# Kernel tuning notes

Measured on AMD Instinct MI355X. Metric: run time of the kernel, lower is better.

## Reference

```python
import jax, jax.numpy as jnp
import numpy as np

NH = 16  # num_heads


def _ln(x, eps=1e-6):
    m = x.mean(-1, keepdims=True)
    v = ((x - m) ** 2).mean(-1, keepdims=True)
    return (x - m) * jax.lax.rsqrt(v + eps)


def _mod(z, sh, sc):
    return z * (1 + sc[:, None, :]) + sh[:, None, :]


def _attn(q, k, v, out_w, out_b, nh=NH):
    B, S, E = q.shape
    hd = E // nh
    q = q.reshape(B, S, nh, hd)
    k = k.reshape(B, -1, nh, hd)
    v = v.reshape(B, -1, nh, hd)
    s = jnp.einsum('bqhd,bkhd->bhqk', q, k) / float(np.sqrt(hd))
    a = jax.nn.softmax(s, axis=-1)
    o = jnp.einsum('bhqk,bkhd->bqhd', a, v).reshape(B, S, E)
    return o @ out_w.T + out_b


def setup_inputs() -> dict:
    key = jax.random.key(0)
    ks = jax.random.split(key, 40)
    E, L, Ne, I, p, C, clip, Kd = 1024, 2, 8, 4096, 2, 4, 768, 1536
    N = (64 // p) ** 2
    n = lambda k, shape, s=0.02: (jax.random.normal(k, shape, jnp.float32) * s)
    inp = {
        'x': jax.random.normal(ks[0], (2, C, 64, 64), jnp.float32),
        't': jax.random.uniform(ks[1], (2,), jnp.float32) * 1000.0,
        'clip_vec': jax.random.normal(ks[2], (2, clip), jnp.float32),
        'qwen_context': jax.random.normal(ks[3], (2, 256, Kd), jnp.float32),
        'conv_w': n(ks[4], (E, C, p, p)),
        'conv_b': n(ks[5], (E,)),
        'pos_embed': n(ks[6], (1, N, E)),
        'tmlp_w1': n(ks[7], (256, 256)), 'tmlp_b1': n(ks[8], (256,)),
        'tmlp_w2': n(ks[9], (256, 256)), 'tmlp_b2': n(ks[10], (256,)),
        'cond_w': n(ks[11], (E, 256 + clip)), 'cond_b': n(ks[12], (E,)),
        'ada_w': n(ks[13], (L, 9 * E, E)), 'ada_b': n(ks[14], (L, 9 * E)),
        'sa_in_w': n(ks[15], (L, 3 * E, E)), 'sa_in_b': n(ks[16], (L, 3 * E)),
        'sa_out_w': n(ks[17], (L, E, E)), 'sa_out_b': n(ks[18], (L, E)),
        'ca_q_w': n(ks[19], (L, E, E)), 'ca_k_w': n(ks[20], (L, E, Kd)),
        'ca_v_w': n(ks[21], (L, E, Kd)), 'ca_in_b': n(ks[22], (L, 3 * E)),
        'ca_out_w': n(ks[23], (L, E, E)), 'ca_out_b': n(ks[24], (L, E)),
        'gate_w': n(ks[25], (L, Ne, E)), 'gate_b': n(ks[26], (L, Ne)),
        'e_w1': n(ks[27], (L, Ne, I, E)), 'e_b1': n(ks[28], (L, Ne, I)),
        'e_w2': n(ks[29], (L, Ne, E, I)), 'e_b2': n(ks[30], (L, Ne, E)),
        'fin_w': n(ks[31], (p * p * C, E)), 'fin_b': n(ks[32], (p * p * C,)),
    }
    return inp


def reference(x, t, clip_vec, qwen_context, conv_w, conv_b, pos_embed,
              tmlp_w1, tmlp_b1, tmlp_w2, tmlp_b2, cond_w, cond_b,
              ada_w, ada_b, sa_in_w, sa_in_b, sa_out_w, sa_out_b,
              ca_q_w, ca_k_w, ca_v_w, ca_in_b, ca_out_w, ca_out_b,
              gate_w, gate_b, e_w1, e_b1, e_w2, e_b2, fin_w, fin_b):
    B, C, H, W = x.shape
    E, p = conv_w.shape[0], conv_w.shape[-1]
    h, w = H // p, W // p
    # patch-embed conv (kernel==stride) as unfold + matmul
    patches = x.reshape(B, C, h, p, w, p).transpose(0, 2, 4, 1, 3, 5).reshape(B, h * w, C * p * p)
    xt = patches @ conv_w.reshape(E, -1).T + conv_b + pos_embed
    # sinusoidal timestep embedding (dim 256)
    half = 128
    freqs = jnp.exp(jnp.arange(half, dtype=jnp.float32) * (-np.log(10000.0) / (half - 1)))
    te = t[:, None] * freqs[None, :]
    te = jnp.concatenate([jnp.sin(te), jnp.cos(te)], -1)
    te = jax.nn.silu(te @ tmlp_w1.T + tmlp_b1) @ tmlp_w2.T + tmlp_b2
    c = jnp.concatenate([te, clip_vec], -1) @ cond_w.T + cond_b  # [B,E]
    depth = ada_w.shape[0]
    for i in range(depth):
        pr = jax.nn.silu(c) @ ada_w[i].T + ada_b[i]
        sh_sa, sc_sa, g_sa, sh_ca, sc_ca, g_ca, sh_m, sc_m, g_m = jnp.split(pr, 9, axis=1)
        # self-attention
        xn = _mod(_ln(xt), sh_sa, sc_sa)
        qkv = xn @ sa_in_w[i].T + sa_in_b[i]
        q, k, v = jnp.split(qkv, 3, axis=-1)
        xt = xt + g_sa[:, None, :] * _attn(q, k, v, sa_out_w[i], sa_out_b[i])
        # cross-attention with separate q/k/v projections
        xn = _mod(_ln(xt), sh_ca, sc_ca)
        q = xn @ ca_q_w[i].T + ca_in_b[i, :E]
        k = qwen_context @ ca_k_w[i].T + ca_in_b[i, E:2 * E]
        v = qwen_context @ ca_v_w[i].T + ca_in_b[i, 2 * E:]
        xt = xt + g_ca[:, None, :] * _attn(q, k, v, ca_out_w[i], ca_out_b[i])
        # top-2 sparse MoE (dense-combine formulation: zero weight for unrouted experts)
        xn = _mod(_ln(xt), sh_m, sc_m)
        probs = jax.nn.softmax(xn @ gate_w[i].T + gate_b[i], axis=-1)
        tw, ti = jax.lax.top_k(probs, 2)
        tw = tw / (tw.sum(-1, keepdims=True) + 1e-6)
        wd = (jax.nn.one_hot(ti, probs.shape[-1], dtype=xn.dtype) * tw[..., None]).sum(-2)  # [B,S,Ne]
        hid = jax.nn.gelu(jnp.einsum('bsd,eid->bsei', xn, e_w1[i]) + e_b1[i], approximate=True)
        y = jnp.einsum('bsei,eoi->bseo', hid, e_w2[i]) + e_b2[i]
        moe = jnp.einsum('bseo,bse->bso', y, wd)
        xt = xt + g_m[:, None, :] * moe
    # final layer + unpatchify (nhwpqc->nchpwq)
    xt = _ln(xt) @ fin_w.T + fin_b
    out = xt.reshape(B, h, w, p, p, C).transpose(0, 5, 1, 3, 2, 4).reshape(B, C, h * p, w * p)
    return out
```

## Files before the change

kernel.cpp:

```cpp
#include <hip/hip_runtime.h>
#include <hip/hip_bf16.h>

#define B_ 2
#define S_ 1024
#define E_ 1024
#define NHEAD 16
#define NE 8
#define II 4096
#define KD 1536
#define CLIP_ 768
#define TOK (B_*S_)
#define NSLOTP 5120

typedef short bf16x8 __attribute__((ext_vector_type(8)));
typedef float f32x4 __attribute__((ext_vector_type(4)));

__device__ __forceinline__ float siluf(float x){ return x/(1.f+expf(-x)); }
__device__ __forceinline__ float geluf(float x){
    float x3 = x*x*x;
    return 0.5f*x*(1.f+tanhf(0.7978845608028654f*(x+0.044715f*x3)));
}
__device__ __forceinline__ unsigned short h16(float x){
    union { __hip_bfloat16 b; unsigned short u; } c;
    c.b = __float2bfloat16(x);
    return c.u;
}
__device__ __forceinline__ unsigned pk2(float a, float b){
    return (unsigned)h16(a) | ((unsigned)h16(b)<<16);
}
__device__ __forceinline__ void sp(float a, unsigned& hb, unsigned& lb){
    unsigned short h = h16(a);
    float r = a - __uint_as_float(((unsigned)h)<<16);
    hb = h; lb = h16(r);
}
__device__ __forceinline__ size_t pidx(int row, int k, int K){
    return (((size_t)(row>>4)*(K>>5) + (k>>5))<<9) + (((k>>3)&3)<<7) + ((row&15)<<3) + (k&7);
}
__device__ __forceinline__ void gload16(const unsigned short* g, unsigned short* l){
    __builtin_amdgcn_global_load_lds((const __attribute__((address_space(1))) void*)g,
                                     (__attribute__((address_space(3))) void*)l, 16, 0, 0);
}

union U8 { unsigned u[4]; bf16x8 v; uint4 q; };

__global__ void k_patch_embed(const float* __restrict__ x, const float* __restrict__ cw,
                              const float* __restrict__ cb, const float* __restrict__ pos,
                              float* __restrict__ xt){
    int token = blockIdx.x;
    int b = token >> 10, n = token & 1023;
    int hh = n >> 5, ww = n & 31;
    __shared__ float patch[16];
    int tid = threadIdx.x;
    if (tid < 16){
        int c = tid >> 2, py = (tid >> 1) & 1, px = tid & 1;
        patch[tid] = x[(((size_t)b*4 + c)*64 + hh*2+py)*64 + ww*2+px];
    }
    __syncthreads();
    for (int e = tid; e < E_; e += 256){
        float acc = cb[e];
        #pragma unroll
        for (int j=0;j<16;j++) acc += patch[j]*cw[e*16+j];
        xt[(size_t)token*E_ + e] = acc + pos[(size_t)n*E_ + e];
    }
}

__global__ void k_time_cond(const float* __restrict__ t, const float* __restrict__ clip,
                            const float* __restrict__ w1, const float* __restrict__ b1,
                            const float* __restrict__ w2, const float* __restrict__ b2,
                            const float* __restrict__ cw, const float* __restrict__ cbias,
                            float* __restrict__ silu_c){
    int b = blockIdx.x, tid = threadIdx.x;
    __shared__ float te[256], h1[256], te2[256];
    if (tid < 128){
        float f = expf((float)tid * (-9.210340371976184f/127.f));
        float a = t[b]*f;
        te[tid]     = sinf(a);
        te[tid+128] = cosf(a);
    }
    __syncthreads();
    {
        float acc = b1[tid];
        const float* wr = w1 + (size_t)tid*256;
        for (int k=0;k<256;k++) acc += te[k]*wr[k];
        h1[tid] = siluf(acc);
    }
    __syncthreads();
    {
        float acc = b2[tid];
        const float* wr = w2 + (size_t)tid*256;
        for (int k=0;k<256;k++) acc += h1[k]*wr[k];
        te2[tid] = acc;
    }
    __syncthreads();
    const float* cl = clip + (size_t)b*CLIP_;
    for (int e = tid; e < E_; e += 256){
        float acc = cbias[e];
        const float* wr = cw + (size_t)e*1024;
        for (int k=0;k<256;k++)  acc += te2[k]*wr[k];
        for (int k=0;k<CLIP_;k++) acc += cl[k]*wr[256+k];
        silu_c[b*E_+e] = siluf(acc);
    }
}

__global__ void k_ada2(const float* __restrict__ sic, const float* __restrict__ aw,
                       const float* __restrict__ ab, float* __restrict__ pr){
    int row = blockIdx.x*4 + (threadIdx.x>>6);
    int lane = threadIdx.x & 63;
    const float* w = aw + (size_t)row*1024;
    float a0 = 0.f, a1 = 0.f;
    #pragma unroll
    for (int it=0; it<4; it++){
        int k = it*256 + lane*4;
        float4 wv = *(const float4*)(w+k);
        float4 x0 = *(const float4*)(sic+k);
        float4 x1 = *(const float4*)(sic+1024+k);
        a0 += wv.x*x0.x + wv.y*x0.y + wv.z*x0.z + wv.w*x0.w;
        a1 += wv.x*x1.x + wv.y*x1.y + wv.z*x1.z + wv.w*x1.w;
    }
    #pragma unroll
    for (int off=32; off; off>>=1){ a0 += __shfl_down(a0,off); a1 += __shfl_down(a1,off); }
    if (lane==0){
        float bb = ab[row];
        pr[row] = a0 + bb;
        pr[9*E_ + row] = a1 + bb;
    }
}

template<int PACK>
__global__ void k_ln_mod(const float* __restrict__ src, float* __restrict__ dst32,
                         unsigned short* __restrict__ dsth, unsigned short* __restrict__ dstl,
                         const float* __restrict__ pr, int shc, int scc){
    int token = blockIdx.x, tid = threadIdx.x;
    int b = token >> 10;
    const float* row = src + (size_t)token*E_;
    float4 v = *(const float4*)(row + tid*4);
    float s = v.x+v.y+v.z+v.w;
    float ss = v.x*v.x+v.y*v.y+v.z*v.z+v.w*v.w;
    #pragma unroll
    for (int off=32; off; off>>=1){ s += __shfl_down(s,off); ss += __shfl_down(ss,off); }
    __shared__ float rs_[4], rss_[4];
    int wid = tid >> 6;
    if ((tid&63)==0){ rs_[wid]=s; rss_[wid]=ss; }
    __syncthreads();
    s  = rs_[0]+rs_[1]+rs_[2]+rs_[3];
    ss = rss_[0]+rss_[1]+rss_[2]+rss_[3];
    float mean = s*(1.f/1024.f);
    float rstd = rsqrtf(ss*(1.f/1024.f) - mean*mean + 1e-6f);
    const float* shv = pr + b*9*E_ + shc*E_;
    const float* scv = pr + b*9*E_ + scc*E_;
    int e = tid*4;
    float o[4];
    float4 sc4 = *(const float4*)(scv+e);
    float4 sh4 = *(const float4*)(shv+e);
    o[0] = (v.x-mean)*rstd*(1.f+sc4.x) + sh4.x;
    o[1] = (v.y-mean)*rstd*(1.f+sc4.y) + sh4.y;
    o[2] = (v.z-mean)*rstd*(1.f+sc4.z) + sh4.z;
    o[3] = (v.w-mean)*rstd*(1.f+sc4.w) + sh4.w;
    unsigned hu[2], lu[2];
    {
        unsigned h0,l0,h1,l1;
        sp(o[0],h0,l0); sp(o[1],h1,l1);
        hu[0]=h0|(h1<<16); lu[0]=l0|(l1<<16);
        sp(o[2],h0,l0); sp(o[3],h1,l1);
        hu[1]=h0|(h1<<16); lu[1]=l0|(l1<<16);
    }
    if (PACK){
        size_t base = pidx(token, e, E_);
        *(uint2*)(dsth + base) = make_uint2(hu[0],hu[1]);
        *(uint2*)(dstl + base) = make_uint2(lu[0],lu[1]);
    } else {
        *(float4*)(dst32 + (size_t)token*E_ + e) = make_float4(o[0],o[1],o[2],o[3]);
        *(uint2*)(dsth + (size_t)token*E_ + e) = make_uint2(hu[0],hu[1]);
        *(uint2*)(dstl + (size_t)token*E_ + e) = make_uint2(lu[0],lu[1]);
    }
}

__global__ void k_pack_qwen(const float* __restrict__ q, unsigned short* __restrict__ hp,
                            unsigned short* __restrict__ lp){
    int r = blockIdx.x;
    int k = threadIdx.x*8;
    float f[8];
    *(float4*)(f+0) = *(const float4*)(q + (size_t)r*KD + k);
    *(float4*)(f+4) = *(const float4*)(q + (size_t)r*KD + k + 4);
    U8 H, L;
    #pragma unroll
    for (int i=0;i<4;i++){
        unsigned h0,l0,h1,l1;
        sp(f[2*i],h0,l0); sp(f[2*i+1],h1,l1);
        H.u[i] = h0|(h1<<16); L.u[i] = l0|(l1<<16);
    }
    size_t dst = pidx(r, k, KD);
    *(uint4*)(hp + dst) = H.q;
    *(uint4*)(lp + dst) = L.q;
}

__global__ void k_gather_pack(const unsigned short* __restrict__ xh,
                              const unsigned short* __restrict__ xl,
                              const int* __restrict__ list,
                              unsigned short* __restrict__ oh, unsigned short* __restrict__ ol){
    int s = blockIdx.x;
    int tid = threadIdx.x;
    int token = list[s];
    int k = tid*8;
    size_t src = (size_t)token*E_ + k;
    size_t dst = pidx(s, k, E_);
    *(uint4*)(oh + dst) = *(const uint4*)(xh + src);
    *(uint4*)(ol + dst) = *(const uint4*)(xl + src);
}

template<int NPL>
__global__ void k_pack_w(const float* __restrict__ W, unsigned short* __restrict__ hp,
                         unsigned short* __restrict__ lp, int K){
    int rg = blockIdx.x;
    int t = threadIdx.x;
    int K32 = K>>5;
    for (int k = t*8; k < K; k += 1024){
        size_t bb = (((size_t)rg*K32 + (k>>5))<<9) + (((k>>3)&3)<<7);
        #pragma unroll 4
        for (int r=0;r<16;r++){
            const float* src = W + (size_t)(rg*16 + r)*K + k;
            float f[8];
            *(float4*)(f)   = *(const float4*)src;
            *(float4*)(f+4) = *(const float4*)(src+4);
            U8 H, L;
            #pragma unroll
            for (int i2=0;i2<4;i2++){
                unsigned h0,l0,h1,l1;
                sp(f[2*i2],h0,l0); sp(f[2*i2+1],h1,l1);
                H.u[i2]=h0|(h1<<16); L.u[i2]=l0|(l1<<16);
            }
            *(uint4*)(hp + bb + (r<<3)) = H.q;
            if (NPL==2) *(uint4*)(lp + bb + (r<<3)) = L.q;
        }
    }
}

template<int MOE, int EPI, int TERMS, int SPLITK=1>
__global__ __launch_bounds__(256) void k_mm(
    const unsigned short* __restrict__ Ah, const unsigned short* __restrict__ Al,
    const unsigned short* __restrict__ Bh, const unsigned short* __restrict__ Bl,
    const float* __restrict__ biasp, int bstride,
    void* __restrict__ Cp, void* __restrict__ Cp2, int ldc,
    int M, int N, int K,
    const float* __restrict__ pr, int gch,
    const int* __restrict__ cnt, const int* __restrict__ offs)
{
    constexpr int NPL = (TERMS==3)?2:1;
    constexpr int NB  = 2*NPL*8;
    constexpr int NBW = NB/4;
    int e  = MOE ? blockIdx.z : 0;
    int Mm = MOE ? cnt[e] : M;
    int bm = blockIdx.y*128;
    if (MOE && bm >= Mm) return;
    int o0 = MOE ? offs[e] : 0;
    int nt = gridDim.x / SPLITK;
    int ntile = blockIdx.x % nt;
    int kc0 = blockIdx.x / nt;
    int bn = ntile*128;
    int K32 = K >> 5;
    int kbeg = kc0*(K/SPLITK), kend = kbeg + K/SPLITK;
    const float* bias = biasp + (size_t)e*bstride;

    __shared__ __align__(16) unsigned short LDm[2][NB*512];

    int tid = threadIdx.x, lane = tid&63, wid = tid>>6;
    int wm = wid>>1, wn = wid&1;
    int fr = lane&15, fr4 = (lane>>4)*4;
    int l8 = lane<<3;
    int a16 = ((MOE? o0:0) + bm) >> 4;
    int b16 = bn >> 4;
    size_t eoff = (size_t)e * N * K;

    const unsigned short* gb[NBW];
    #pragma unroll
    for (int i=0;i<NBW;i++){
        int bidx = wid*NBW + i;
        int isB = (bidx >= NPL*8) ? 1 : 0;
        int r = bidx - isB*NPL*8;
        int pl = r>>3, rg = r&7;
        const unsigned short* p;
        size_t rgg;
        if (!isB){ p = (TERMS==3 && pl)? Al : Ah; rgg = (size_t)(a16 + rg); }
        else     { p = ((TERMS==3 && pl)? Bl : Bh) + eoff; rgg = (size_t)(b16 + rg); }
        gb[i] = p + ((rgg*K32)<<9) + l8;
    }

    f32x4 acc[4][4];
    #pragma unroll
    for (int m=0;m<4;m++)
        #pragma unroll
        for (int n=0;n<4;n++) acc[m][n] = (f32x4){0.f,0.f,0.f,0.f};

    {
        int kc = kbeg>>5;
        #pragma unroll
        for (int i=0;i<NBW;i++)
            gload16(gb[i] + ((size_t)kc<<9), &LDm[0][(size_t)(wid*NBW+i)<<9]);
    }
    __syncthreads();
    int cur = 0;
    for (int k0=kbeg; k0<kend; k0+=32){
        bool nxt = (k0+32) < kend;
        if (nxt){
            int kc = (k0+32)>>5;
            #pragma unroll
            for (int i=0;i<NBW;i++)
                gload16(gb[i] + ((size_t)kc<<9), &LDm[cur^1][(size_t)(wid*NBW+i)<<9]);
        }
        bf16x8 ah[4], al[4], bh[4], bl[4];
        #pragma unroll
        for (int m=0;m<4;m++){
            ah[m] = *(const bf16x8*)&LDm[cur][(size_t)((wm*4+m)<<9) + l8];
            if (TERMS==3) al[m] = *(const bf16x8*)&LDm[cur][(size_t)((8+wm*4+m)<<9) + l8];
        }
        #pragma unroll
        for (int n=0;n<4;n++){
            bh[n] = *(const bf16x8*)&LDm[cur][(size_t)((NPL*8 + wn*4+n)<<9) + l8];
            if (TERMS==3) bl[n] = *(const bf16x8*)&LDm[cur][(size_t)((NPL*8+8 + wn*4+n)<<9) + l8];
        }
        #pragma unroll
        for (int m=0;m<4;m++)
            #pragma unroll
            for (int n=0;n<4;n++){
                acc[m][n] = __builtin_amdgcn_mfma_f32_16x16x32_bf16(ah[m], bh[n], acc[m][n], 0, 0, 0);
                if (TERMS==3){
                    acc[m][n] = __builtin_amdgcn_mfma_f32_16x16x32_bf16(ah[m], bl[n], acc[m][n], 0, 0, 0);
                    acc[m][n] = __builtin_amdgcn_mfma_f32_16x16x32_bf16(al[m], bh[n], acc[m][n], 0, 0, 0);
                }
            }
        __syncthreads();
        cur ^= 1;
    }

    #pragma unroll
    for (int m=0;m<4;m++){
        #pragma unroll
        for (int j=0;j<4;j++){
            int row = bm + wm*64 + m*16 + fr4 + j;
            if (EPI != 2 && row >= Mm) continue;
            #pragma unroll
            for (int n=0;n<4;n++){
                int col = bn + wn*64 + n*16 + fr;
                float bv = (SPLITK==1 || kc0==0) ? bias[col] : 0.f;
                float v = acc[m][n][j] + bv;
                if (EPI==0){
                    ((float*)Cp)[(size_t)row*ldc + col] = v;
                } else if (EPI==1){
                    int bb = row >> 10;
                    ((float*)Cp)[(size_t)row*ldc + col] += pr[bb*9*E_ + gch*E_ + col] * v;
                } else if (EPI==2){
                    size_t pi = pidx(o0 + row, col, II);
                    if (TERMS==3){
                        unsigned hb, lb; sp(geluf(v), hb, lb);
                        ((unsigned short*)Cp )[pi] = (unsigned short)hb;
                        ((unsigned short*)Cp2)[pi] = (unsigned short)lb;
                    } else {
                        ((unsigned short*)Cp )[pi] = h16(geluf(v));
                    }
                } else {
                    if (SPLITK==1)
                        ((float*)Cp)[(size_t)(o0+row)*ldc + col] = v;
                    else
                        atomicAdd(&((float*)Cp)[(size_t)(o0+row)*ldc + col], v);
                }
            }
        }
    }
}

__global__ __launch_bounds__(256) void k_attn_m(
    const float* __restrict__ qp, int qstride,
    const float* __restrict__ kp, const float* __restrict__ vp, int kvstride,
    unsigned short* __restrict__ oph, unsigned short* __restrict__ opl,
    int Sq, int Sk, float scale)
{
    __shared__ __align__(16) unsigned short Kh[64*72];
    __shared__ __align__(16) unsigned short Kl[64*72];
    __shared__ __align__(16) unsigned V_i[64*70];
    __shared__ __align__(16) unsigned short P_[4][2][16*72];

    int tid = threadIdx.x, lane = tid & 63, wid = tid >> 6;
    int g = lane >> 4, fr = lane & 15;
    int h = blockIdx.y, b = blockIdx.z;
    int qbase = blockIdx.x*64;

    bf16x8 qh[2], ql[2];
    {
        const float* qr = qp + (size_t)(b*Sq + qbase + wid*16 + fr)*qstride + h*64;
        #pragma unroll
        for (int ds=0; ds<2; ds++){
            float f[8];
            *(float4*)(f+0) = *(const float4*)(qr + ds*32 + g*8);
            *(float4*)(f+4) = *(const float4*)(qr + ds*32 + g*8 + 4);
            U8 uh, ul;
            #pragma unroll
            for (int i=0;i<4;i++){
                unsigned h0,l0,h1,l1;
                sp(f[2*i]*scale, h0,l0); sp(f[2*i+1]*scale, h1,l1);
                uh.u[i] = h0|(h1<<16); ul.u[i] = l0|(l1<<16);
            }
            qh[ds] = uh.v; ql[ds] = ul.v;
        }
    }

    float m_run = -1e30f, l_run = 0.f;
    f32x4 oacc[4];
    #pragma unroll
    for (int dt=0;dt<4;dt++) oacc[dt] = (f32x4){0.f,0.f,0.f,0.f};

    unsigned short* PhW = &P_[wid][0][0];
    unsigned short* PlW = &P_[wid][1][0];

    for (int kt0 = 0; kt0 < Sk; kt0 += 64){
        __syncthreads();
        {
            int srow = tid >> 2, d0 = (tid & 3) << 4;
            size_t grow = (size_t)(b*Sk + kt0 + srow)*kvstride + h*64 + d0;
            {
                const float* srcp = kp + grow;
                float f[16];
                *(float4*)(f+0)  = *(const float4*)(srcp+0);
                *(float4*)(f+4)  = *(const float4*)(srcp+4);
                *(float4*)(f+8)  = *(const float4*)(srcp+8);
                *(float4*)(f+12) = *(const float4*)(srcp+12);
                U8 uh0, uh1, ul0, ul1;
                #pragma unroll
                for (int i=0;i<4;i++){
                    unsigned a0,b0,a1,b1;
                    sp(f[2*i],a0,b0); sp(f[2*i+1],a1,b1);
                    uh0.u[i] = a0|(a1<<16); ul0.u[i] = b0|(b1<<16);
                }
                #pragma unroll
                for (int i=0;i<4;i++){
                    unsigned a0,b0,a1,b1;
                    sp(f[8+2*i],a0,b0); sp(f[8+2*i+1],a1,b1);
                    uh1.u[i] = a0|(a1<<16); ul1.u[i] = b0|(b1<<16);
                }
                int base = srow*72 + d0;
                *(uint4*)&Kh[base]     = uh0.q;
                *(uint4*)&Kh[base + 8] = uh1.q;
                *(uint4*)&Kl[base]     = ul0.q;
                *(uint4*)&Kl[base + 8] = ul1.q;
            }
            {
                const float* srcp = vp + grow;
                float f[16];
                *(float4*)(f+0)  = *(const float4*)(srcp+0);
                *(float4*)(f+4)  = *(const float4*)(srcp+4);
                *(float4*)(f+8)  = *(const float4*)(srcp+8);
                *(float4*)(f+12) = *(const float4*)(srcp+12);
                int base = srow*70 + d0;
                #pragma unroll
                for (int i4=0;i4<4;i4++){
                    U8 u;
                    #pragma unroll
                    for (int i=0;i<4;i++){
                        unsigned hb, lb; sp(f[4*i4+i], hb, lb);
                        u.u[i] = hb | (lb<<16);
                    }
                    *(uint2*)&V_i[base + i4*4]     = make_uint2(u.u[0], u.u[1]);
                    *(uint2*)&V_i[base + i4*4 + 2] = make_uint2(u.u[2], u.u[3]);
                }
            }
        }
        __syncthreads();

        f32x4 st[4];
        #pragma unroll
        for (int kt=0;kt<4;kt++) st[kt] = (f32x4){0.f,0.f,0.f,0.f};
        #pragma unroll
        for (int ds=0; ds<2; ds++){
            #pragma unroll
            for (int kt=0;kt<4;kt++){
                int row = kt*16 + fr;
                int so = row*72 + ds*32 + g*8;
                bf16x8 kh  = *(const bf16x8*)&Kh[so];
                bf16x8 klo = *(const bf16x8*)&Kl[so];
                st[kt] = __builtin_amdgcn_mfma_f32_16x16x32_bf16(kh, qh[ds], st[kt], 0,0,0);
                st[kt] = __builtin_amdgcn_mfma_f32_16x16x32_bf16(kh, ql[ds], st[kt], 0,0,0);
                st[kt] = __builtin_amdgcn_mfma_f32_16x16x32_bf16(klo, qh[ds], st[kt], 0,0,0);
            }
        }

        float pmax = -1e30f;
        #pragma unroll
        for (int kt=0;kt<4;kt++)
            #pragma unroll
            for (int r=0;r<4;r++) pmax = fmaxf(pmax, st[kt][r]);
        pmax = fmaxf(pmax, __shfl_xor(pmax, 16));
        pmax = fmaxf(pmax, __shfl_xor(pmax, 32));
        float mnew = fmaxf(m_run, pmax);
        float p[4][4]; float psum = 0.f;
        #pragma unroll
        for (int kt=0;kt<4;kt++)
            #pragma unroll
            for (int r=0;r<4;r++){ float pv = expf(st[kt][r] - mnew); p[kt][r] = pv; psum += pv; }
        psum += __shfl_xor(psum, 16);
        psum += __shfl_xor(psum, 32);
        float corr = expf(m_run - mnew);
        l_run = l_run*corr + psum;
        m_run = mnew;
        #pragma unroll
        for (int j=0;j<4;j++){
            float cj = __shfl(corr, g*4 + j);
            #pragma unroll
            for (int dt=0;dt<4;dt++) oacc[dt][j] *= cj;
        }

        #pragma unroll
        for (int kt=0;kt<4;kt++){
            unsigned h0,l0,h1,l1,h2,l2,h3,l3;
            sp(p[kt][0],h0,l0); sp(p[kt][1],h1,l1);
            sp(p[kt][2],h2,l2); sp(p[kt][3],h3,l3);
            int base = fr*72 + kt*16 + g*4;
            *(unsigned*)&PhW[base]     = h0|(h1<<16);
            *(unsigned*)&PhW[base + 2] = h2|(h3<<16);
            *(unsigned*)&PlW[base]     = l0|(l1<<16);
            *(unsigned*)&PlW[base + 2] = l2|(l3<<16);
        }

        #pragma unroll
        for (int ks=0; ks<2; ks++){
            int pso = fr*72 + ks*32 + g*8;
            bf16x8 ph = *(const bf16x8*)&PhW[pso];
            bf16x8 pl = *(const bf16x8*)&PlW[pso];
            #pragma unroll
            for (int dt=0; dt<4; dt++){
                unsigned w[8];
                #pragma unroll
                for (int j=0;j<8;j++){
                    int row = ks*32 + g*8 + j;
                    w[j] = V_i[row*70 + dt*16 + fr];
                }
                U8 vh, vl;
                #pragma unroll
                for (int i=0;i<4;i++){
                    vh.u[i] = (w[2*i] & 0xffffu) | (w[2*i+1] << 16);
                    vl.u[i] = (w[2*i] >> 16)     | (w[2*i+1] & 0xffff0000u);
                }
                oacc[dt] = __builtin_amdgcn_mfma_f32_16x16x32_bf16(ph, vh.v, oacc[dt], 0,0,0);
                oacc[dt] = __builtin_amdgcn_mfma_f32_16x16x32_bf16(ph, vl.v, oacc[dt], 0,0,0);
                oacc[dt] = __builtin_amdgcn_mfma_f32_16x16x32_bf16(pl, vh.v, oacc[dt], 0,0,0);
            }
        }
    }

    float linv = 1.f / l_run;
    #pragma unroll
    for (int j=0;j<4;j++){
        float lj = __shfl(linv, g*4 + j);
        int row = b*Sq + qbase + wid*16 + g*4 + j;
        #pragma unroll
        for (int dt=0;dt<4;dt++){
            unsigned hb, lb; sp(oacc[dt][j]*lj, hb, lb);
            int k = h*64 + dt*16 + fr;
            size_t pi = pidx(row, k, E_);
            oph[pi] = (unsigned short)hb;
            opl[pi] = (unsigned short)lb;
        }
    }
}

__global__ void k_route(const float* __restrict__ xn, const float* __restrict__ gw,
                        const float* __restrict__ gb, int* __restrict__ i01,
                        float* __restrict__ w01, int* __restrict__ cnt){
    int token = blockIdx.x, lane = threadIdx.x;
    const float* row = xn + (size_t)token*E_;
    float part[8] = {0,0,0,0,0,0,0,0};
    for (int k = lane; k < E_; k += 64){
        float xv = row[k];
        #pragma unroll
        for (int e=0;e<8;e++) part[e] += xv*gw[e*E_+k];
    }
    #pragma unroll
    for (int e=0;e<8;e++){
        #pragma unroll
        for (int off=32; off; off>>=1) part[e] += __shfl_down(part[e], off);
    }
    if (lane==0){
        float lg[8]; float mx = -1e30f;
        #pragma unroll
        for (int e=0;e<8;e++){ lg[e] = part[e]+gb[e]; if (lg[e]>mx) mx = lg[e]; }
        float sum = 0.f;
        #pragma unroll
        for (int e=0;e<8;e++){ lg[e] = expf(lg[e]-mx); sum += lg[e]; }
        int a0 = 0;
        #pragma unroll
        for (int e=1;e<8;e++) if (lg[e] > lg[a0]) a0 = e;
        int a1 = (a0==0)?1:0;
        #pragma unroll
        for (int e=0;e<8;e++) if (e!=a0 && lg[e] > lg[a1]) a1 = e;
        float p0 = lg[a0]/sum, p1 = lg[a1]/sum;
        float inv = 1.f/(p0+p1+1e-6f);
        i01[token*2+0]=a0; i01[token*2+1]=a1;
        w01[token*2+0]=p0*inv; w01[token*2+1]=p1*inv;
        atomicAdd(&cnt[a0],1); atomicAdd(&cnt[a1],1);
    }
}

__global__ void k_scan(const int* __restrict__ cnt, int* __restrict__ offs, int* __restrict__ curs){
    if (threadIdx.x==0 && blockIdx.x==0){
        int o = 0;
        for (int e=0;e<8;e++){
            offs[e]=o; curs[e]=o;
            o += ((cnt[e]+127)>>7)<<7;
        }
    }
}

__global__ void k_place(const int* __restrict__ i01,
                        int* __restrict__ curs, int* __restrict__ list,
                        int* __restrict__ t2s){
    int t = blockIdx.x*256 + threadIdx.x;
    if (t >= TOK) return;
    #pragma unroll
    for (int s=0;s<2;s++){
        int e = i01[t*2+s];
        int p = atomicAdd(&curs[e],1);
        list[p] = t;
        t2s[t*2+s] = p;
    }
}

__global__ void k_moe_combine2(float* __restrict__ xt, const float* __restrict__ yslot,
                               const int* __restrict__ t2s, const float* __restrict__ w01,
                               const float* __restrict__ pr){
    int idx = blockIdx.x*256 + threadIdx.x;
    int token = idx >> 10, n = idx & 1023;
    int b = token >> 10;
    int s0 = t2s[token*2], s1 = t2s[token*2+1];
    float mo = w01[token*2]*yslot[(size_t)s0*E_+n] + w01[token*2+1]*yslot[(size_t)s1*E_+n];
    xt[idx] += pr[b*9*E_ + 8*E_ + n]*mo;
}

__global__ void k_final(const float* __restrict__ xt, const float* __restrict__ fw,
                        const float* __restrict__ fb, float* __restrict__ out){
    int token = blockIdx.x, tid = threadIdx.x;
    int b = token >> 10, n = token & 1023, hh = n >> 5, ww = n & 31;
    const float* row = xt + (size_t)token*E_;
    float4 v = *(const float4*)(row + tid*4);
    float s = v.x+v.y+v.z+v.w;
    float ss = v.x*v.x+v.y*v.y+v.z*v.z+v.w*v.w;
    #pragma unroll
    for (int off=32; off; off>>=1){ s += __shfl_down(s,off); ss += __shfl_down(ss,off); }
    __shared__ float rs_[4], rss_[4];
    int wid = tid >> 6;
    if ((tid&63)==0){ rs_[wid]=s; rss_[wid]=ss; }
    __syncthreads();
    s  = rs_[0]+rs_[1]+rs_[2]+rs_[3];
    ss = rss_[0]+rss_[1]+rss_[2]+rss_[3];
    float mean = s*(1.f/1024.f);
    float rstd = rsqrtf(ss*(1.f/1024.f) - mean*mean + 1e-6f);
    __shared__ float xl[1024];
    int e = tid*4;
    xl[e+0]=(v.x-mean)*rstd; xl[e+1]=(v.y-mean)*rstd;
    xl[e+2]=(v.z-mean)*rstd; xl[e+3]=(v.w-mean)*rstd;
    __syncthreads();
    int o = tid & 15, seg = tid >> 4;
    float part = 0.f;
    const float* wr = fw + (size_t)o*E_ + seg*64;
    const float* xr = xl + seg*64;
    #pragma unroll 8
    for (int j=0;j<64;j++) part += xr[j]*wr[j];
    __shared__ float ps[16][17];
    ps[seg][o] = part;
    __syncthreads();
    if (tid < 16){
        float acc = fb[tid];
        #pragma unroll
        for (int s2=0;s2<16;s2++) acc += ps[s2][tid];
        int py = tid>>3, px = (tid>>2)&1, ch = tid&3;
        out[(((size_t)b*4+ch)*64 + hh*2+py)*64 + ww*2+px] = acc;
    }
}

extern "C" void kernel_launch(void* const* d_in, const int* in_sizes, int n_in,
                              void* d_out, int out_size, void* d_ws, size_t ws_size,
                              hipStream_t stream){
    const float* x        = (const float*)d_in[0];
    const float* t        = (const float*)d_in[1];
    const float* clip     = (const float*)d_in[2];
    const float* qwen     = (const float*)d_in[3];
    const float* conv_w   = (const float*)d_in[4];
    const float* conv_b   = (const float*)d_in[5];
    const float* pos      = (const float*)d_in[6];
    const float* tw1      = (const float*)d_in[7];
    const float* tb1      = (const float*)d_in[8];
    const float* tw2      = (const float*)d_in[9];
    const float* tb2      = (const float*)d_in[10];
    const float* cond_w   = (const float*)d_in[11];
    const float* cond_b   = (const float*)d_in[12];
    const float* ada_w    = (const float*)d_in[13];
    const float* ada_b    = (const float*)d_in[14];
    const float* sa_in_w  = (const float*)d_in[15];
    const float* sa_in_b  = (const float*)d_in[16];
    const float* sa_out_w = (const float*)d_in[17];
    const float* sa_out_b = (const float*)d_in[18];
    const float* ca_q_w   = (const float*)d_in[19];
    const float* ca_k_w   = (const float*)d_in[20];
    const float* ca_v_w   = (const float*)d_in[21];
    const float* ca_in_b  = (const float*)d_in[22];
    const float* ca_out_w = (const float*)d_in[23];
    const float* ca_out_b = (const float*)d_in[24];
    const float* gate_w   = (const float*)d_in[25];
    const float* gate_b   = (const float*)d_in[26];
    const float* e_w1     = (const float*)d_in[27];
    const float* e_b1     = (const float*)d_in[28];
    const float* e_w2     = (const float*)d_in[29];
    const float* e_b2     = (const float*)d_in[30];
    const float* fin_w    = (const float*)d_in[31];
    const float* fin_b    = (const float*)d_in[32];

    float* ws    = (float*)d_ws;
    float* xt    = ws;
    float* xn    = ws + 2097152;
    float* qkv   = ws + 4194304;
    float* yslot = qkv;
    unsigned short* xnh  = (unsigned short*)(ws + 10485760);
    unsigned short* xnl  = (unsigned short*)(ws + 11534336);
    unsigned short* obh  = (unsigned short*)(ws + 12582912);
    unsigned short* obl  = (unsigned short*)(ws + 13631488);
    unsigned short* xnsh = (unsigned short*)(ws + 14680064);
    unsigned short* xnsl = (unsigned short*)(ws + 17301504);
    unsigned short* hidh = (unsigned short*)(ws + 19922944);
    unsigned short* hidl = (unsigned short*)(ws + 30408704);
    unsigned short* qwph = (unsigned short*)(ws + 40894464);
    unsigned short* qwpl = (unsigned short*)(ws + 41287680);
    float* kbuf  = ws + 41680896;
    float* vbuf  = ws + 42205184;
    float* pr    = ws + 42729472;
    float* sic   = ws + 42747904;
    float* w01   = ws + 42749952;
    int*   i01   = (int*)(ws + 42754048);
    int*   t2s   = (int*)(ws + 42758144);
    int*   list  = (int*)(ws + 42762240);
    int*   cnt   = (int*)(ws + 42767360);
    int*   offs  = cnt + 8;
    int*   curs  = cnt + 16;
    unsigned short* wb = (unsigned short*)(ws + 42768384);

    const size_t SA_IN_H=0, SA_IN_L=3145728, SA_OUT_H=6291456, SA_OUT_L=7340032;
    const size_t CAQ_H=8388608, CAQ_L=9437184, CAK_H=10485760, CAK_L=12058624;
    const size_t CAV_H=13631488, CAV_L=15204352, CAO_H=16777216, CAO_L=17825792;
    const size_t W_H=0, W_L=16777216;

    k_patch_embed<<<TOK,256,0,stream>>>(x, conv_w, conv_b, pos, xt);
    k_time_cond<<<B_,256,0,stream>>>(t, clip, tw1, tb1, tw2, tb2, cond_w, cond_b, sic);
    k_pack_qwen<<<B_*256,192,0,stream>>>(qwen, qwph, qwpl);

    for (int i=0;i<2;i++){
        k_ada2<<<2304,256,0,stream>>>(sic, ada_w + (size_t)i*9*E_*E_,
                                      ada_b + (size_t)i*9*E_, pr);
        k_pack_w<2><<<192,128,0,stream>>>(sa_in_w + (size_t)i*3*E_*E_, wb+SA_IN_H, wb+SA_IN_L, E_);
        k_pack_w<2><<<64,128,0,stream>>>(sa_out_w + (size_t)i*E_*E_, wb+SA_OUT_H, wb+SA_OUT_L, E_);
        k_pack_w<2><<<64,128,0,stream>>>(ca_q_w + (size_t)i*E_*E_, wb+CAQ_H, wb+CAQ_L, E_);
        k_pack_w<2><<<64,128,0,stream>>>(ca_k_w + (size_t)i*E_*KD, wb+CAK_H, wb+CAK_L, KD);
        k_pack_w<2><<<64,128,0,stream>>>(ca_v_w + (size_t)i*E_*KD, wb+CAV_H, wb+CAV_L, KD);
        k_pack_w<2><<<64,128,0,stream>>>(ca_out_w + (size_t)i*E_*E_, wb+CAO_H, wb+CAO_L, E_);
        k_ln_mod<1><<<TOK,256,0,stream>>>(xt, nullptr, xnh, xnl, pr, 0, 1);
        k_mm<0,0,3><<<dim3(24,16),256,0,stream>>>(
            xnh, xnl, wb+SA_IN_H, wb+SA_IN_L, sa_in_b + (size_t)i*3*E_, 0,
            qkv, nullptr, 3*E_, TOK, 3*E_, E_, nullptr, 0, nullptr, nullptr);
        k_attn_m<<<dim3(16,NHEAD,B_),256,0,stream>>>(qkv, 3*E_, qkv+E_, qkv+2*E_, 3*E_,
                                                     obh, obl, S_, S_, 0.125f);
        k_mm<0,1,3><<<dim3(8,16),256,0,stream>>>(
            obh, obl, wb+SA_OUT_H, wb+SA_OUT_L, sa_out_b + (size_t)i*E_, 0,
            xt, nullptr, E_, TOK, E_, E_, pr, 2, nullptr, nullptr);
        k_ln_mod<1><<<TOK,256,0,stream>>>(xt, nullptr, xnh, xnl, pr, 3, 4);
        k_mm<0,0,3><<<dim3(8,16),256,0,stream>>>(
            xnh, xnl, wb+CAQ_H, wb+CAQ_L, ca_in_b + (size_t)i*3*E_, 0,
            qkv, nullptr, E_, TOK, E_, E_, nullptr, 0, nullptr, nullptr);
        k_mm<0,0,3><<<dim3(8,4),256,0,stream>>>(
            qwph, qwpl, wb+CAK_H, wb+CAK_L, ca_in_b + (size_t)i*3*E_ + E_, 0,
            kbuf, nullptr, E_, B_*256, E_, KD, nullptr, 0, nullptr, nullptr);
        k_mm<0,0,3><<<dim3(8,4),256,0,stream>>>(
            qwph, qwpl, wb+CAV_H, wb+CAV_L, ca_in_b + (size_t)i*3*E_ + 2*E_, 0,
            vbuf, nullptr, E_, B_*256, E_, KD, nullptr, 0, nullptr, nullptr);
        k_attn_m<<<dim3(16,NHEAD,B_),256,0,stream>>>(qkv, E_, kbuf, vbuf, E_,
                                                     obh, obl, S_, 256, 0.125f);
        k_mm<0,1,3><<<dim3(8,16),256,0,stream>>>(
            obh, obl, wb+CAO_H, wb+CAO_L, ca_out_b + (size_t)i*E_, 0,
            xt, nullptr, E_, TOK, E_, E_, pr, 5, nullptr, nullptr);
        k_ln_mod<0><<<TOK,256,0,stream>>>(xt, xn, xnh, xnl, pr, 6, 7);
        hipMemsetAsync(cnt, 0, 8*sizeof(int), stream);
        hipMemsetAsync(list, 0, NSLOTP*sizeof(int), stream);
        k_route<<<TOK,64,0,stream>>>(xn, gate_w + (size_t)i*NE*E_, gate_b + (size_t)i*NE,
                                     i01, w01, cnt);
        k_scan<<<1,64,0,stream>>>(cnt, offs, curs);
        k_place<<<TOK/256,256,0,stream>>>(i01, curs, list, t2s);
        k_gather_pack<<<NSLOTP,128,0,stream>>>(xnh, xnl, list, xnsh, xnsl);
        hipMemsetAsync(yslot, 0, (size_t)NSLOTP*E_*sizeof(float), stream);
        for (int e0=0;e0<NE;e0+=4){
            if (i==0){
                k_pack_w<2><<<1024,128,0,stream>>>(e_w1 + ((size_t)i*NE+e0)*II*E_, wb+W_H, wb+W_L, E_);
                k_mm<1,2,3><<<dim3(32,32,4),256,0,stream>>>(
                    xnsh, xnsl, wb+W_H, wb+W_L, e_b1 + (size_t)i*NE*II + (size_t)e0*II, II,
                    hidh, hidl, II, 0, II, E_, nullptr, 0, cnt+e0, offs+e0);
            } else {
                k_pack_w<1><<<1024,128,0,stream>>>(e_w1 + ((size_t)i*NE+e0)*II*E_, wb+W_H, nullptr, E_);
                k_mm<1,2,1><<<dim3(32,32,4),256,0,stream>>>(
                    xnsh, nullptr, wb+W_H, nullptr, e_b1 + (size_t)i*NE*II + (size_t)e0*II, II,
                    hidh, nullptr, II, 0, II, E_, nullptr, 0, cnt+e0, offs+e0);
            }
        }
        for (int e0=0;e0<NE;e0+=4){
            if (i==0){
                k_pack_w<2><<<256,128,0,stream>>>(e_w2 + ((size_t)i*NE+e0)*E_*II, wb+W_H, wb+W_L, II);
                k_mm<1,3,3,4><<<dim3(32,32,4),256,0,stream>>>(
                    hidh, hidl, wb+W_H, wb+W_L, e_b2 + (size_t)i*NE*E_ + (size_t)e0*E_, E_,
                    yslot, nullptr, E_, 0, E_, II, nullptr, 0, cnt+e0, offs+e0);
            } else {
                k_pack_w<1><<<256,128,0,stream>>>(e_w2 + ((size_t)i*NE+e0)*E_*II, wb+W_H, nullptr, II);
                k_mm<1,3,1,4><<<dim3(32,32,4),256,0,stream>>>(
                    hidh, nullptr, wb+W_H, nullptr, e_b2 + (size_t)i*NE*E_ + (size_t)e0*E_, E_,
                    yslot, nullptr, E_, 0, E_, II, nullptr, 0, cnt+e0, offs+e0);
            }
        }
        k_moe_combine2<<<TOK*E_/256,256,0,stream>>>(xt, yslot, t2s, w01, pr);
    }
    k_final<<<TOK,256,0,stream>>>(xt, fin_w, fin_b, (float*)d_out);
}
```

Before: 2.407 ms.

## Emit attention K/V pre-split in head-major layout from GEMM epilogues

The QKV and cross-attention K/V projection GEMMs now write K and V directly as hi/lo bf16 splits in a per-head contiguous layout through new epilogues. The attention kernel then loads them with plain vector copies instead of converting fp32 rows on every tile load. The conditioning matvec moves out of a 2-block kernel into a wave-per-output kernel with many blocks. The layer-1 MoE launches all 8 experts in one pack plus one GEMM per stage instead of two chunks. The cost is a larger packed-weight buffer and more complex epilogue index math.

```diff
diff --git a/kernel.cpp b/kernel.cpp
--- a/kernel.cpp
+++ b/kernel.cpp
@@ -64,13 +64,12 @@
     }
 }
 
-__global__ void k_time_cond(const float* __restrict__ t, const float* __restrict__ clip,
-                            const float* __restrict__ w1, const float* __restrict__ b1,
-                            const float* __restrict__ w2, const float* __restrict__ b2,
-                            const float* __restrict__ cw, const float* __restrict__ cbias,
-                            float* __restrict__ silu_c){
+__global__ void k_time_mlp(const float* __restrict__ t,
+                           const float* __restrict__ w1, const float* __restrict__ b1,
+                           const float* __restrict__ w2, const float* __restrict__ b2,
+                           float* __restrict__ te2g){
     int b = blockIdx.x, tid = threadIdx.x;
-    __shared__ float te[256], h1[256], te2[256];
+    __shared__ float te[256], h1[256];
     if (tid < 128){
         float f = expf((float)tid * (-9.210340371976184f/127.f));
         float a = t[b]*f;
@@ -89,17 +88,25 @@
         float acc = b2[tid];
         const float* wr = w2 + (size_t)tid*256;
         for (int k=0;k<256;k++) acc += h1[k]*wr[k];
-        te2[tid] = acc;
-    }
-    __syncthreads();
-    const float* cl = clip + (size_t)b*CLIP_;
-    for (int e = tid; e < E_; e += 256){
-        float acc = cbias[e];
-        const float* wr = cw + (size_t)e*1024;
-        for (int k=0;k<256;k++)  acc += te2[k]*wr[k];
-        for (int k=0;k<CLIP_;k++) acc += cl[k]*wr[256+k];
-        silu_c[b*E_+e] = siluf(acc);
-    }
+        te2g[b*256+tid] = acc;
+    }
+}
+
+__global__ void k_cond(const float* __restrict__ te2g, const float* __restrict__ clip,
+                       const float* __restrict__ cw, const float* __restrict__ cb,
+                       float* __restrict__ silu_c){
+    int idx = blockIdx.x*4 + (threadIdx.x>>6);
+    int lane = threadIdx.x & 63;
+    int b = idx >> 10, e = idx & 1023;
+    const float* wr = cw + (size_t)e*1024;
+    float acc = 0.f;
+    for (int k=lane; k<1024; k+=64){
+        float xv = (k<256)? te2g[b*256+k] : clip[b*CLIP_ + k-256];
+        acc += xv*wr[k];
+    }
+    #pragma unroll
+    for (int off=32; off; off>>=1) acc += __shfl_down(acc,off);
+    if (lane==0) silu_c[b*E_+e] = siluf(acc + cb[e]);
 }
 
 __global__ void k_ada2(const float* __restrict__ sic, const float* __restrict__ aw,
@@ -240,8 +247,8 @@
     const unsigned short* __restrict__ Ah, const unsigned short* __restrict__ Al,
     const unsigned short* __restrict__ Bh, const unsigned short* __restrict__ Bl,
     const float* __restrict__ biasp, int bstride,
-    void* __restrict__ Cp, void* __restrict__ Cp2, int ldc,
-    int M, int N, int K,
+    void* __restrict__ Cp, void* __restrict__ Cp2, void* __restrict__ Cp3, void* __restrict__ Cp4,
+    int ldc, int M, int N, int K,
     const float* __restrict__ pr, int gch,
     const int* __restrict__ cnt, const int* __restrict__ offs)
 {
@@ -357,11 +364,39 @@
                     } else {
                         ((unsigned short*)Cp )[pi] = h16(geluf(v));
                     }
-                } else {
+                } else if (EPI==3){
                     if (SPLITK==1)
                         ((float*)Cp)[(size_t)(o0+row)*ldc + col] = v;
                     else
                         atomicAdd(&((float*)Cp)[(size_t)(o0+row)*ldc + col], v);
+                } else if (EPI==4){
+                    if (col < 1024){
+                        ((float*)Cp)[(size_t)row*1024 + col] = v;
+                    } else {
+                        int c2 = col - 1024;
+                        int isv = c2 >> 10;
+                        int cc = c2 & 1023;
+                        int hh2 = cc >> 6, d = cc & 63;
+                        size_t idx = (((size_t)(row>>10)*NHEAD + hh2)*1024 + (row & 1023))*64 + d;
+                        unsigned hb, lb; sp(v, hb, lb);
+                        if (!isv){
+                            ((unsigned short*)Cp2)[idx] = (unsigned short)hb;
+                            ((unsigned short*)Cp3)[idx] = (unsigned short)lb;
+                        } else {
+                            ((unsigned*)Cp4)[idx] = hb | (lb<<16);
+                        }
+                    }
+                } else if (EPI==5){
+                    int hh2 = col >> 6, d = col & 63;
+                    size_t idx = (((size_t)(row>>8)*NHEAD + hh2)*256 + (row & 255))*64 + d;
+                    unsigned hb, lb; sp(v, hb, lb);
+                    ((unsigned short*)Cp )[idx] = (unsigned short)hb;
+                    ((unsigned short*)Cp2)[idx] = (unsigned short)lb;
+                } else {
+                    int hh2 = col >> 6, d = col & 63;
+                    size_t idx = (((size_t)(row>>8)*NHEAD + hh2)*256 + (row & 255))*64 + d;
+                    unsigned hb, lb; sp(v, hb, lb);
+                    ((unsigned*)Cp)[idx] = hb | (lb<<16);
                 }
             }
         }
@@ -370,7 +405,8 @@
 
 __global__ __launch_bounds__(256) void k_attn_m(
     const float* __restrict__ qp, int qstride,
-    const float* __restrict__ kp, const float* __restrict__ vp, int kvstride,
+    const unsigned short* __restrict__ Khp, const unsigned short* __restrict__ Klp,
+    const unsigned* __restrict__ Vip,
     unsigned short* __restrict__ oph, unsigned short* __restrict__ opl,
     int Sq, int Sk, float scale)
 {
@@ -383,6 +419,7 @@
     int g = lane >> 4, fr = lane & 15;
     int h = blockIdx.y, b = blockIdx.z;
     int qbase = blockIdx.x*64;
+    size_t bhbase = (size_t)(b*NHEAD + h)*Sk*64;
 
     bf16x8 qh[2], ql[2];
     {
@@ -415,52 +452,19 @@
         __syncthreads();
         {
             int srow = tid >> 2, d0 = (tid & 3) << 4;
-            size_t grow = (size_t)(b*Sk + kt0 + srow)*kvstride + h*64 + d0;
-            {
-                const float* srcp = kp + grow;
-                float f[16];
-                *(float4*)(f+0)  = *(const float4*)(srcp+0);
-                *(float4*)(f+4)  = *(const float4*)(srcp+4);
-                *(float4*)(f+8)  = *(const float4*)(srcp+8);
-                *(float4*)(f+12) = *(const float4*)(srcp+12);
-                U8 uh0, uh1, ul0, ul1;
-                #pragma unroll
-                for (int i=0;i<4;i++){
-                    unsigned a0,b0,a1,b1;
-                    sp(f[2*i],a0,b0); sp(f[2*i+1],a1,b1);
-                    uh0.u[i] = a0|(a1<<16); ul0.u[i] = b0|(b1<<16);
-                }
-                #pragma unroll
-                for (int i=0;i<4;i++){
-                    unsigned a0,b0,a1,b1;
-                    sp(f[8+2*i],a0,b0); sp(f[8+2*i+1],a1,b1);
-                    uh1.u[i] = a0|(a1<<16); ul1.u[i] = b0|(b1<<16);
-                }
-                int base = srow*72 + d0;
-                *(uint4*)&Kh[base]     = uh0.q;
-                *(uint4*)&Kh[base + 8] = uh1.q;
-                *(uint4*)&Kl[base]     = ul0.q;
-                *(uint4*)&Kl[base + 8] = ul1.q;
-            }
-            {
-                const float* srcp = vp + grow;
-                float f[16];
-                *(float4*)(f+0)  = *(const float4*)(srcp+0);
-                *(float4*)(f+4)  = *(const float4*)(srcp+4);
-                *(float4*)(f+8)  = *(const float4*)(srcp+8);
-                *(float4*)(f+12) = *(const float4*)(srcp+12);
-                int base = srow*70 + d0;
-                #pragma unroll
-                for (int i4=0;i4<4;i4++){
-                    U8 u;
-                    #pragma unroll
-                    for (int i=0;i<4;i++){
-                        unsigned hb, lb; sp(f[4*i4+i], hb, lb);
-                        u.u[i] = hb | (lb<<16);
-                    }
-                    *(uint2*)&V_i[base + i4*4]     = make_uint2(u.u[0], u.u[1]);
-                    *(uint2*)&V_i[base + i4*4 + 2] = make_uint2(u.u[2], u.u[3]);
-                }
+            size_t gidx = bhbase + (size_t)(kt0 + srow)*64 + d0;
+            int base = srow*72 + d0;
+            *(uint4*)&Kh[base]   = *(const uint4*)(Khp + gidx);
+            *(uint4*)&Kh[base+8] = *(const uint4*)(Khp + gidx + 8);
+            *(uint4*)&Kl[base]   = *(const uint4*)(Klp + gidx);
+            *(uint4*)&Kl[base+8] = *(const uint4*)(Klp + gidx + 8);
+            const unsigned* vsrc = Vip + gidx;
+            int vb = srow*70 + d0;
+            #pragma unroll
+            for (int i4=0;i4<4;i4++){
+                uint4 u = *(const uint4*)(vsrc + i4*4);
+                *(uint2*)&V_i[vb + i4*4]     = make_uint2(u.x,u.y);
+                *(uint2*)&V_i[vb + i4*4 + 2] = make_uint2(u.z,u.w);
             }
         }
         __syncthreads();
@@ -714,8 +718,11 @@
     float* ws    = (float*)d_ws;
     float* xt    = ws;
     float* xn    = ws + 2097152;
-    float* qkv   = ws + 4194304;
-    float* yslot = qkv;
+    float* qbuf  = ws + 4194304;
+    unsigned short* Khp = (unsigned short*)(ws + 6291456);
+    unsigned short* Klp = (unsigned short*)(ws + 7340032);
+    unsigned*       Vip = (unsigned*)(ws + 8388608);
+    float* yslot = ws + 4194304;
     unsigned short* xnh  = (unsigned short*)(ws + 10485760);
     unsigned short* xnl  = (unsigned short*)(ws + 11534336);
     unsigned short* obh  = (unsigned short*)(ws + 12582912);
@@ -726,8 +733,6 @@
     unsigned short* hidl = (unsigned short*)(ws + 30408704);
     unsigned short* qwph = (unsigned short*)(ws + 40894464);
     unsigned short* qwpl = (unsigned short*)(ws + 41287680);
-    float* kbuf  = ws + 41680896;
-    float* vbuf  = ws + 42205184;
     float* pr    = ws + 42729472;
     float* sic   = ws + 42747904;
     float* w01   = ws + 42749952;
@@ -737,6 +742,7 @@
     int*   cnt   = (int*)(ws + 42767360);
     int*   offs  = cnt + 8;
     int*   curs  = cnt + 16;
+    float* te2g  = ws + 42767872;
     unsigned short* wb = (unsigned short*)(ws + 42768384);
 
     const size_t SA_IN_H=0, SA_IN_L=3145728, SA_OUT_H=6291456, SA_OUT_L=7340032;
@@ -745,7 +751,8 @@
     const size_t W_H=0, W_L=16777216;
 
     k_patch_embed<<<TOK,256,0,stream>>>(x, conv_w, conv_b, pos, xt);
-    k_time_cond<<<B_,256,0,stream>>>(t, clip, tw1, tb1, tw2, tb2, cond_w, cond_b, sic);
+    k_time_mlp<<<B_,256,0,stream>>>(t, tw1, tb1, tw2, tb2, te2g);
+    k_cond<<<512,256,0,stream>>>(te2g, clip, cond_w, cond_b, sic);
     k_pack_qwen<<<B_*256,192,0,stream>>>(qwen, qwph, qwpl);
 
     for (int i=0;i<2;i++){
@@ -758,29 +765,29 @@
         k_pack_w<2><<<64,128,0,stream>>>(ca_v_w + (size_t)i*E_*KD, wb+CAV_H, wb+CAV_L, KD);
         k_pack_w<2><<<64,128,0,stream>>>(ca_out_w + (size_t)i*E_*E_, wb+CAO_H, wb+CAO_L, E_);
         k_ln_mod<1><<<TOK,256,0,stream>>>(xt, nullptr, xnh, xnl, pr, 0, 1);
-        k_mm<0,0,3><<<dim3(24,16),256,0,stream>>>(
+        k_mm<0,4,3><<<dim3(24,16),256,0,stream>>>(
             xnh, xnl, wb+SA_IN_H, wb+SA_IN_L, sa_in_b + (size_t)i*3*E_, 0,
-            qkv, nullptr, 3*E_, TOK, 3*E_, E_, nullptr, 0, nullptr, nullptr);
-        k_attn_m<<<dim3(16,NHEAD,B_),256,0,stream>>>(qkv, 3*E_, qkv+E_, qkv+2*E_, 3*E_,
+            qbuf, Khp, Klp, Vip, 0, TOK, 3*E_, E_, nullptr, 0, nullptr, nullptr);
+        k_attn_m<<<dim3(16,NHEAD,B_),256,0,stream>>>(qbuf, E_, Khp, Klp, Vip,
                                                      obh, obl, S_, S_, 0.125f);
         k_mm<0,1,3><<<dim3(8,16),256,0,stream>>>(
             obh, obl, wb+SA_OUT_H, wb+SA_OUT_L, sa_out_b + (size_t)i*E_, 0,
-            xt, nullptr, E_, TOK, E_, E_, pr, 2, nullptr, nullptr);
+            xt, nullptr, nullptr, nullptr, E_, TOK, E_, E_, pr, 2, nullptr, nullptr);
         k_ln_mod<1><<<TOK,256,0,stream>>>(xt, nullptr, xnh, xnl, pr, 3, 4);
         k_mm<0,0,3><<<dim3(8,16),256,0,stream>>>(
             xnh, xnl, wb+CAQ_H, wb+CAQ_L, ca_in_b + (size_t)i*3*E_, 0,
-            qkv, nullptr, E_, TOK, E_, E_, nullptr, 0, nullptr, nullptr);
-        k_mm<0,0,3><<<dim3(8,4),256,0,stream>>>(
+            qbuf, nullptr, nullptr, nullptr, E_, TOK, E_, E_, nullptr, 0, nullptr, nullptr);
+        k_mm<0,5,3><<<dim3(8,4),256,0,stream>>>(
             qwph, qwpl, wb+CAK_H, wb+CAK_L, ca_in_b + (size_t)i*3*E_ + E_, 0,
-            kbuf, nullptr, E_, B_*256, E_, KD, nullptr, 0, nullptr, nullptr);
-        k_mm<0,0,3><<<dim3(8,4),256,0,stream>>>(
+            Khp, Klp, nullptr, nullptr, 0, B_*256, E_, KD, nullptr, 0, nullptr, nullptr);
+        k_mm<0,6,3><<<dim3(8,4),256,0,stream>>>(
             qwph, qwpl, wb+CAV_H, wb+CAV_L, ca_in_b + (size_t)i*3*E_ + 2*E_, 0,
-            vbuf, nullptr, E_, B_*256, E_, KD, nullptr, 0, nullptr, nullptr);
-        k_attn_m<<<dim3(16,NHEAD,B_),256,0,stream>>>(qkv, E_, kbuf, vbuf, E_,
+            Vip, nullptr, nullptr, nullptr, 0, B_*256, E_, KD, nullptr, 0, nullptr, nullptr);
+        k_attn_m<<<dim3(16,NHEAD,B_),256,0,stream>>>(qbuf, E_, Khp, Klp, Vip,
                                                      obh, obl, S_, 256, 0.125f);
         k_mm<0,1,3><<<dim3(8,16),256,0,stream>>>(
             obh, obl, wb+CAO_H, wb+CAO_L, ca_out_b + (size_t)i*E_, 0,
-            xt, nullptr, E_, TOK, E_, E_, pr, 5, nullptr, nullptr);
+            xt, nullptr, nullptr, nullptr, E_, TOK, E_, E_, pr, 5, nullptr, nullptr);
         k_ln_mod<0><<<TOK,256,0,stream>>>(xt, xn, xnh, xnl, pr, 6, 7);
         hipMemsetAsync(cnt, 0, 8*sizeof(int), stream);
         hipMemsetAsync(list, 0, NSLOTP*sizeof(int), stream);
@@ -790,31 +797,28 @@
         k_place<<<TOK/256,256,0,stream>>>(i01, curs, list, t2s);
         k_gather_pack<<<NSLOTP,128,0,stream>>>(xnh, xnl, list, xnsh, xnsl);
         hipMemsetAsync(yslot, 0, (size_t)NSLOTP*E_*sizeof(float), stream);
-        for (int e0=0;e0<NE;e0+=4){
-            if (i==0){
+        if (i==0){
+            for (int e0=0;e0<NE;e0+=4){
                 k_pack_w<2><<<1024,128,0,stream>>>(e_w1 + ((size_t)i*NE+e0)*II*E_, wb+W_H, wb+W_L, E_);
                 k_mm<1,2,3><<<dim3(32,32,4),256,0,stream>>>(
                     xnsh, xnsl, wb+W_H, wb+W_L, e_b1 + (size_t)i*NE*II + (size_t)e0*II, II,
-                    hidh, hidl, II, 0, II, E_, nullptr, 0, cnt+e0, offs+e0);
-            } else {
-                k_pack_w<1><<<1024,128,0,stream>>>(e_w1 + ((size_t)i*NE+e0)*II*E_, wb+W_H, nullptr, E_);
-                k_mm<1,2,1><<<dim3(32,32,4),256,0,stream>>>(
-                    xnsh, nullptr, wb+W_H, nullptr, e_b1 + (size_t)i*NE*II + (size_t)e0*II, II,
-                    hidh, nullptr, II, 0, II, E_, nullptr, 0, cnt+e0, offs+e0);
+                    hidh, hidl, nullptr, nullptr, II, 0, II, E_, nullptr, 0, cnt+e0, offs+e0);
             }
-        }
-        for (int e0=0;e0<NE;e0+=4){
-            if (i==0){
+            for (int e0=0;e0<NE;e0+=4){
                 k_pack_w<2><<<256,128,0,stream>>>(e_w2 + ((size_t)i*NE+e0)*E_*II, wb+W_H, wb+W_L, II);
                 k_mm<1,3,3,4><<<dim3(32,32,4),256,0,stream>>>(
                     hidh, hidl, wb+W_H, wb+W_L, e_b2 + (size_t)i*NE*E_ + (size_t)e0*E_, E_,
-                    yslot, nullptr, E_, 0, E_, II, nullptr, 0, cnt+e0, offs+e0);
-            } else {
-                k_pack_w<1><<<256,128,0,stream>>>(e_w2 + ((size_t)i*NE+e0)*E_*II, wb+W_H, nullptr, II);
-                k_mm<1,3,1,4><<<dim3(32,32,4),256,0,stream>>>(
-                    hidh, nullptr, wb+W_H, nullptr, e_b2 + (size_t)i*NE*E_ + (size_t)e0*E_, E_,
-                    yslot, nullptr, E_, 0, E_, II, nullptr, 0, cnt+e0, offs+e0);
+                    yslot, nullptr, nullptr, nullptr, E_, 0, E_, II, nullptr, 0, cnt+e0, offs+e0);
             }
+        } else {
+            k_pack_w<1><<<2048,128,0,stream>>>(e_w1 + (size_t)i*NE*II*E_, wb+W_H, nullptr, E_);
+            k_mm<1,2,1><<<dim3(32,32,NE),256,0,stream>>>(
+                xnsh, nullptr, wb+W_H, nullptr, e_b1 + (size_t)i*NE*II, II,
+                hidh, nullptr, nullptr, nullptr, II, 0, II, E_, nullptr, 0, cnt, offs);
+            k_pack_w<1><<<512,128,0,stream>>>(e_w2 + (size_t)i*NE*E_*II, wb+W_H, nullptr, II);
+            k_mm<1,3,1,4><<<dim3(32,32,NE),256,0,stream>>>(
+                hidh, nullptr, wb+W_H, nullptr, e_b2 + (size_t)i*NE*E_, E_,
+                yslot, nullptr, nullptr, nullptr, E_, 0, E_, II, nullptr, 0, cnt, offs);
         }
         k_moe_combine2<<<TOK*E_/256,256,0,stream>>>(xt, yslot, t2s, w01, pr);
     }
```

Result: faster. 2.319 ms (-3.7%).
